# Kernel optimization log

Hardware: AMD Instinct MI355X
Metric: run time of the kernel (lower is better)

The kernel has to match this reference:

```python
import jax, jax.numpy as jnp
import numpy as np

N = 20000        # total nodes in batched graph
E = 160000       # edges (avg in-degree 8)
D_IN = 512
D_OUT = 512
MAX_DEG = 10
BN_EPS = 1e-5


def setup_inputs() -> dict:
    key = jax.random.key(0)
    ks = jax.random.split(key, 8)
    feats = jax.random.normal(ks[0], (N, D_IN), dtype=jnp.float32)
    src = jax.random.randint(ks[1], (E,), 0, N)
    dst = jax.random.randint(ks[2], (E,), 0, N)
    # Wl[d], bl[d]: lins_l for degree d (d>=1); Wl[0] is never used since h==0 for deg-0 nodes.
    # Wr[0], bl[0] play the role of lin_zero_deg; Wr[d] (d>=1) are the bias-free lins_r.
    Wl = jax.random.normal(ks[3], (MAX_DEG + 1, D_IN, D_OUT), dtype=jnp.float32) * 0.02
    Wr = jax.random.normal(ks[4], (MAX_DEG + 1, D_IN, D_OUT), dtype=jnp.float32) * 0.02
    bl = jax.random.normal(ks[5], (MAX_DEG + 1, D_OUT), dtype=jnp.float32) * 0.02
    gamma = jnp.ones((D_OUT,), dtype=jnp.float32)
    beta = jnp.zeros((D_OUT,), dtype=jnp.float32)
    return {"feats": feats, "src": src, "dst": dst, "Wl": Wl, "Wr": Wr,
            "bl": bl, "gamma": gamma, "beta": beta}


def reference(feats, src, dst, Wl, Wr, bl, gamma, beta):
    # 1) neighbor sum: h[v] = sum_{(u->v) in E} feats[u]   (fn.copy_u + fn.sum)
    h = jax.ops.segment_sum(feats[src], dst, num_segments=N)  # [N, D_IN]
    # in-degrees, clamped to max_degree
    deg = jnp.clip(jax.ops.segment_sum(jnp.ones((E,), dtype=jnp.int32), dst,
                                       num_segments=N), 0, MAX_DEG)  # [N]
    # 2) degree-bucketed linears, vectorized over the 11 buckets then gathered per node.
    #    out[n] = h[n] @ Wl[deg[n]] + feats[n] @ Wr[deg[n]] + bl[deg[n]]
    #    deg==0 nodes have h==0, so this reduces to lin_zero_deg(feats) = feats@Wr[0]+bl[0].
    Hl = jnp.einsum('ni,dio->dno', h, Wl)      # [11, N, D_OUT]
    Hr = jnp.einsum('ni,dio->dno', feats, Wr)  # [11, N, D_OUT]
    out = (Hl + Hr + bl[:, None, :])[deg, jnp.arange(N)]  # [N, D_OUT]
    # 3) batchnorm (training mode: batch stats, biased variance)
    mean = out.mean(axis=0)
    var = out.var(axis=0)
    out = (out - mean) * jax.lax.rsqrt(var + BN_EPS) * gamma + beta
    # 4) max aggregation over graph with self loops (fn.copy_u + fn.max)
    self_ids = jnp.arange(N)
    src_s = jnp.concatenate([src, self_ids])
    dst_s = jnp.concatenate([dst, self_ids])
    out = jax.ops.segment_max(out[src_s], dst_s, num_segments=N)  # [N, D_OUT]
    return out
```

## Files before the change

### kernel.cpp

```cpp
#include <hip/hip_runtime.h>
#include <hip/hip_bf16.h>
#include <stdint.h>

#define N_NODES 20000
#define N_EDGES 160000
#define DIN 512
#define DOUT 512
#define NBUCKET 11
#define KDIM 1024
#define MAXTILES 168
#define BN_EPS 1e-5f
#define CAP 64
#define CAST_BLOCKS (N_NODES / 4)
#define WT_BLOCKS ((KDIM / 32) * (DOUT / 32) * NBUCKET)
#define BUCKET_BLOCKS ((N_NODES + 255) / 256)

typedef float f32x4 __attribute__((ext_vector_type(4)));
typedef __attribute__((ext_vector_type(8))) __bf16 bf16x8;

static __device__ __forceinline__ unsigned short f2bf(float f) {
    union { float f; unsigned u; } v; v.f = f;
    unsigned r = v.u + 0x7FFFu + ((v.u >> 16) & 1u);
    return (unsigned short)(r >> 16);
}
static __device__ __forceinline__ float bflo(unsigned p) {
    union { unsigned u; float f; } v; v.u = p << 16; return v.f;
}
static __device__ __forceinline__ float bfhi(unsigned p) {
    union { unsigned u; float f; } v; v.u = p & 0xFFFF0000u; return v.f;
}
static __device__ __forceinline__ unsigned packbf(float lo, float hi) {
    return (unsigned)f2bf(lo) | ((unsigned)f2bf(hi) << 16);
}

static __device__ __forceinline__ void gload_lds16(const unsigned short* g, unsigned short* l) {
    __builtin_amdgcn_global_load_lds(
        (const __attribute__((address_space(1))) unsigned int*)g,
        (__attribute__((address_space(3))) unsigned int*)l, 16, 0, 0);
}

__global__ void k_scatter(const int* __restrict__ src, const int* __restrict__ dst,
                          int* __restrict__ cursor, int* __restrict__ eidx2) {
    int e = blockIdx.x * 256 + threadIdx.x;
    if (e >= N_EDGES) return;
    int v = dst[e];
    int slot = atomicAdd(&cursor[v], 1);
    if (slot < CAP) eidx2[v * CAP + slot] = src[e];
}

__global__ __launch_bounds__(256)
void k_prep(const float* __restrict__ feats, const float* __restrict__ Wl,
            const float* __restrict__ Wr, const int* __restrict__ cursor,
            unsigned short* __restrict__ X, unsigned short* __restrict__ Wt,
            int* __restrict__ bucket_cnt, int* __restrict__ bucket_nodes) {
    int b = blockIdx.x;
    int t = threadIdx.x;
    if (b < CAST_BLOCKS) {
        int n = b * 4 + (t >> 6);
        int col = (t & 63) * 8;
        f32x4 a = *(const f32x4*)(feats + (size_t)n * DIN + col);
        f32x4 c = *(const f32x4*)(feats + (size_t)n * DIN + col + 4);
        uint4 p;
        p.x = packbf(a[0], a[1]); p.y = packbf(a[2], a[3]);
        p.z = packbf(c[0], c[1]); p.w = packbf(c[2], c[3]);
        *(uint4*)(X + (size_t)n * KDIM + DIN + col) = p;
        return;
    }
    if (b < CAST_BLOCKS + WT_BLOCKS) {
        __shared__ float tile[32][33];
        int idx = b - CAST_BLOCKS;
        int d = idx / (32 * 16);
        int rem = idx % (32 * 16);
        int k0 = (rem & 31) * 32;
        int n0 = (rem >> 5) * 32;
        int c = t & 31, r0 = t >> 5;
        const float* srcp = (k0 < DIN) ? (Wl + (size_t)d * DIN * DOUT)
                                       : (Wr + (size_t)d * DIN * DOUT - (size_t)DIN * DOUT);
        for (int rr = 0; rr < 4; ++rr) {
            int r = r0 + rr * 8;
            tile[r][c] = srcp[(size_t)(k0 + r) * DOUT + n0 + c];
        }
        __syncthreads();
        for (int rr = 0; rr < 4; ++rr) {
            int r = r0 + rr * 8;
            Wt[((size_t)d * DOUT + n0 + r) * KDIM + k0 + c] = f2bf(tile[c][r]);
        }
        return;
    }
    __shared__ int lhist[NBUCKET];
    __shared__ int lbase[NBUCKET];
    if (t < NBUCKET) lhist[t] = 0;
    __syncthreads();
    int v = (b - CAST_BLOCKS - WT_BLOCKS) * 256 + t;
    int d = -1, slot = 0;
    if (v < N_NODES) {
        d = min(cursor[v], NBUCKET - 1);
        slot = atomicAdd(&lhist[d], 1);
    }
    __syncthreads();
    if (t < NBUCKET && lhist[t] > 0) lbase[t] = atomicAdd(&bucket_cnt[t], lhist[t]);
    __syncthreads();
    if (v < N_NODES) bucket_nodes[d * N_NODES + lbase[d] + slot] = v;
}

__global__ __launch_bounds__(256)
void k_build_x(const int* __restrict__ eidx2, const int* __restrict__ cursor,
               unsigned short* __restrict__ X) {
    int n = blockIdx.x * 4 + (threadIdx.x >> 6);
    int lane = threadIdx.x & 63;
    int col = lane * 8;
    int e = min(cursor[n], CAP);
    int av = eidx2[(size_t)n * CAP + lane];
    float acc[8] = {0,0,0,0,0,0,0,0};
    int i = 0;
    for (; i + 7 < e; i += 8) {
        uint4 p[8];
#pragma unroll
        for (int j = 0; j < 8; ++j) {
            int u = __shfl(av, i + j, 64);
            p[j] = *(const uint4*)(X + (size_t)u * KDIM + DIN + col);
        }
#pragma unroll
        for (int j = 0; j < 8; ++j) {
            acc[0] += bflo(p[j].x); acc[1] += bfhi(p[j].x);
            acc[2] += bflo(p[j].y); acc[3] += bfhi(p[j].y);
            acc[4] += bflo(p[j].z); acc[5] += bfhi(p[j].z);
            acc[6] += bflo(p[j].w); acc[7] += bfhi(p[j].w);
        }
    }
    if (i + 3 < e) {
        uint4 p[4];
#pragma unroll
        for (int j = 0; j < 4; ++j) {
            int u = __shfl(av, i + j, 64);
            p[j] = *(const uint4*)(X + (size_t)u * KDIM + DIN + col);
        }
#pragma unroll
        for (int j = 0; j < 4; ++j) {
            acc[0] += bflo(p[j].x); acc[1] += bfhi(p[j].x);
            acc[2] += bflo(p[j].y); acc[3] += bfhi(p[j].y);
            acc[4] += bflo(p[j].z); acc[5] += bfhi(p[j].z);
            acc[6] += bflo(p[j].w); acc[7] += bfhi(p[j].w);
        }
        i += 4;
    }
    for (; i < e; ++i) {
        int u = __shfl(av, i, 64);
        uint4 p = *(const uint4*)(X + (size_t)u * KDIM + DIN + col);
        acc[0] += bflo(p.x); acc[1] += bfhi(p.x); acc[2] += bflo(p.y); acc[3] += bfhi(p.y);
        acc[4] += bflo(p.z); acc[5] += bfhi(p.z); acc[6] += bflo(p.w); acc[7] += bfhi(p.w);
    }
    uint4 o;
    o.x = packbf(acc[0], acc[1]); o.y = packbf(acc[2], acc[3]);
    o.z = packbf(acc[4], acc[5]); o.w = packbf(acc[6], acc[7]);
    *(uint4*)(X + (size_t)n * KDIM + col) = o;
}

__global__ __launch_bounds__(256)
void k_gemm(const unsigned short* __restrict__ X, const unsigned short* __restrict__ Wt,
            const int* __restrict__ bucket_nodes, const int* __restrict__ bucket_cnt,
            const float* __restrict__ bl, unsigned short* __restrict__ out_pre,
            float* __restrict__ bn_sum, float* __restrict__ bn_sumsq) {
    int idx = blockIdx.x;
    int d = -1, m0 = 0, accum = 0, cnt = 0;
    for (int b = 0; b < NBUCKET; ++b) {
        int c = bucket_cnt[b];
        int nt = (c + 127) >> 7;
        if (d < 0 && idx < accum + nt) { d = b; m0 = (idx - accum) * 128; cnt = c; }
        accum += nt;
    }
    if (d < 0) return;
    int n0 = blockIdx.y * 128;

    __shared__ __align__(16) unsigned short As[128 * 64];
    __shared__ __align__(16) unsigned short Bs[128 * 64];
    __shared__ int ridS[128];
    __shared__ float colsum[128], colsq[128];

    int t = threadIdx.x;
    if (t < 128) {
        int gm = m0 + t;
        ridS[t] = (gm < cnt) ? bucket_nodes[d * N_NODES + gm] : -1;
        colsum[t] = 0.f; colsq[t] = 0.f;
    }
    __syncthreads();

    int lane = t & 63, w = t >> 6;
    int r = lane >> 3;
    int s = lane & 7;
    int sg = s ^ r;

    const unsigned short* gA[4];
    const unsigned short* gB[4];
    unsigned short* lA[4];
    unsigned short* lB[4];
#pragma unroll
    for (int j = 0; j < 4; ++j) {
        int row = w * 32 + j * 8 + r;
        int rid = max(ridS[row], 0);
        gA[j] = X + (size_t)rid * KDIM + sg * 8;
        gB[j] = Wt + ((size_t)d * DOUT + n0 + row) * KDIM + sg * 8;
        lA[j] = &As[(w * 32 + j * 8) * 64];
        lB[j] = &Bs[(w * 32 + j * 8) * 64];
    }

    int wm = (w & 1) * 64, wn = (w >> 1) * 64;
    int lm = lane & 15, q = lane >> 4;
    int sw = lm & 7;

    f32x4 acc[4][4];
#pragma unroll
    for (int i = 0; i < 4; ++i)
#pragma unroll
        for (int j = 0; j < 4; ++j) acc[i][j] = (f32x4){0, 0, 0, 0};

    for (int kt = 0; kt < KDIM / 64; ++kt) {
#pragma unroll
        for (int j = 0; j < 4; ++j) {
            gload_lds16(gA[j] + kt * 64, lA[j]);
            gload_lds16(gB[j] + kt * 64, lB[j]);
        }
        __syncthreads();

#pragma unroll
        for (int kk = 0; kk < 2; ++kk) {
            int slot = (kk * 4 + q) ^ sw;
            bf16x8 af[4], bfr[4];
#pragma unroll
            for (int mt = 0; mt < 4; ++mt)
                af[mt] = *(bf16x8*)&As[(wm + mt * 16 + lm) * 64 + slot * 8];
#pragma unroll
            for (int nt = 0; nt < 4; ++nt)
                bfr[nt] = *(bf16x8*)&Bs[(wn + nt * 16 + lm) * 64 + slot * 8];
#pragma unroll
            for (int mt = 0; mt < 4; ++mt)
#pragma unroll
                for (int nt = 0; nt < 4; ++nt)
                    acc[mt][nt] = __builtin_amdgcn_mfma_f32_16x16x32_bf16(af[mt], bfr[nt], acc[mt][nt], 0, 0, 0);
        }
        __syncthreads();
    }

    const float* blr = bl + d * DOUT + n0;
    float vsum[4] = {0, 0, 0, 0}, vsq[4] = {0, 0, 0, 0};
#pragma unroll
    for (int mt = 0; mt < 4; ++mt) {
#pragma unroll
        for (int rr = 0; rr < 4; ++rr) {
            int row = wm + mt * 16 + q * 4 + rr;
            int grow = ridS[row];
            if (grow < 0) continue;
            unsigned short* orow = out_pre + (size_t)grow * DOUT + n0;
#pragma unroll
            for (int nt = 0; nt < 4; ++nt) {
                int col = wn + nt * 16 + lm;
                float v = acc[mt][nt][rr] + blr[col];
                orow[col] = f2bf(v);
                vsum[nt] += v; vsq[nt] += v * v;
            }
        }
    }
#pragma unroll
    for (int nt = 0; nt < 4; ++nt) {
        vsum[nt] += __shfl_xor(vsum[nt], 16, 64);
        vsum[nt] += __shfl_xor(vsum[nt], 32, 64);
        vsq[nt]  += __shfl_xor(vsq[nt], 16, 64);
        vsq[nt]  += __shfl_xor(vsq[nt], 32, 64);
    }
    if (q == 0) {
#pragma unroll
        for (int nt = 0; nt < 4; ++nt) {
            atomicAdd(&colsum[wn + nt * 16 + lm], vsum[nt]);
            atomicAdd(&colsq[wn + nt * 16 + lm], vsq[nt]);
        }
    }
    __syncthreads();
    if (t < 128) {
        atomicAdd(&bn_sum[n0 + t], colsum[t]);
        atomicAdd(&bn_sumsq[n0 + t], colsq[t]);
    }
}

__global__ __launch_bounds__(256)
void k_max(const unsigned short* __restrict__ out_pre, const int* __restrict__ eidx2,
           const int* __restrict__ cursor, const float* __restrict__ bn_sum,
           const float* __restrict__ bn_sumsq, const float* __restrict__ gamma,
           const float* __restrict__ beta, float* __restrict__ out) {
    int n = blockIdx.x * 4 + (threadIdx.x >> 6);
    int lane = threadIdx.x & 63;
    int col = lane * 8;
    int e = min(cursor[n], CAP);
    int av = eidx2[(size_t)n * CAP + lane];
    float mx[8];
    {
        uint4 p = *(const uint4*)(out_pre + (size_t)n * DOUT + col);
        mx[0] = bflo(p.x); mx[1] = bfhi(p.x); mx[2] = bflo(p.y); mx[3] = bfhi(p.y);
        mx[4] = bflo(p.z); mx[5] = bfhi(p.z); mx[6] = bflo(p.w); mx[7] = bfhi(p.w);
    }
    int i = 0;
    for (; i + 7 < e; i += 8) {
        uint4 p[8];
#pragma unroll
        for (int j = 0; j < 8; ++j) {
            int u = __shfl(av, i + j, 64);
            p[j] = *(const uint4*)(out_pre + (size_t)u * DOUT + col);
        }
#pragma unroll
        for (int j = 0; j < 8; ++j) {
            mx[0] = fmaxf(mx[0], bflo(p[j].x)); mx[1] = fmaxf(mx[1], bfhi(p[j].x));
            mx[2] = fmaxf(mx[2], bflo(p[j].y)); mx[3] = fmaxf(mx[3], bfhi(p[j].y));
            mx[4] = fmaxf(mx[4], bflo(p[j].z)); mx[5] = fmaxf(mx[5], bfhi(p[j].z));
            mx[6] = fmaxf(mx[6], bflo(p[j].w)); mx[7] = fmaxf(mx[7], bfhi(p[j].w));
        }
    }
    if (i + 3 < e) {
        uint4 p[4];
#pragma unroll
        for (int j = 0; j < 4; ++j) {
            int u = __shfl(av, i + j, 64);
            p[j] = *(const uint4*)(out_pre + (size_t)u * DOUT + col);
        }
#pragma unroll
        for (int j = 0; j < 4; ++j) {
            mx[0] = fmaxf(mx[0], bflo(p[j].x)); mx[1] = fmaxf(mx[1], bfhi(p[j].x));
            mx[2] = fmaxf(mx[2], bflo(p[j].y)); mx[3] = fmaxf(mx[3], bfhi(p[j].y));
            mx[4] = fmaxf(mx[4], bflo(p[j].z)); mx[5] = fmaxf(mx[5], bfhi(p[j].z));
            mx[6] = fmaxf(mx[6], bflo(p[j].w)); mx[7] = fmaxf(mx[7], bfhi(p[j].w));
        }
        i += 4;
    }
    for (; i < e; ++i) {
        int u = __shfl(av, i, 64);
        uint4 p = *(const uint4*)(out_pre + (size_t)u * DOUT + col);
        mx[0] = fmaxf(mx[0], bflo(p.x)); mx[1] = fmaxf(mx[1], bfhi(p.x));
        mx[2] = fmaxf(mx[2], bflo(p.y)); mx[3] = fmaxf(mx[3], bfhi(p.y));
        mx[4] = fmaxf(mx[4], bflo(p.z)); mx[5] = fmaxf(mx[5], bfhi(p.z));
        mx[6] = fmaxf(mx[6], bflo(p.w)); mx[7] = fmaxf(mx[7], bfhi(p.w));
    }
    const float inv_n = 1.0f / (float)N_NODES;
    f32x4 sm0 = *(const f32x4*)(bn_sum + col);
    f32x4 sm1 = *(const f32x4*)(bn_sum + col + 4);
    f32x4 sq0 = *(const f32x4*)(bn_sumsq + col);
    f32x4 sq1 = *(const f32x4*)(bn_sumsq + col + 4);
    f32x4 g0 = *(const f32x4*)(gamma + col);
    f32x4 g1 = *(const f32x4*)(gamma + col + 4);
    f32x4 b0 = *(const f32x4*)(beta + col);
    f32x4 b1 = *(const f32x4*)(beta + col + 4);
    f32x4 r0, r1;
#pragma unroll
    for (int jj = 0; jj < 4; ++jj) {
        float mean = sm0[jj] * inv_n;
        float var = sq0[jj] * inv_n - mean * mean;
        float sc = g0[jj] * rsqrtf(var + BN_EPS);
        r0[jj] = mx[jj] * sc + (b0[jj] - mean * sc);
    }
#pragma unroll
    for (int jj = 0; jj < 4; ++jj) {
        float mean = sm1[jj] * inv_n;
        float var = sq1[jj] * inv_n - mean * mean;
        float sc = g1[jj] * rsqrtf(var + BN_EPS);
        r1[jj] = mx[jj + 4] * sc + (b1[jj] - mean * sc);
    }
    *(f32x4*)(out + (size_t)n * DOUT + col) = r0;
    *(f32x4*)(out + (size_t)n * DOUT + col + 4) = r1;
}

extern "C" void kernel_launch(void* const* d_in, const int* in_sizes, int n_in,
                              void* d_out, int out_size, void* d_ws, size_t ws_size,
                              hipStream_t stream) {
    const float* feats = (const float*)d_in[0];
    const int*   src   = (const int*)d_in[1];
    const int*   dst   = (const int*)d_in[2];
    const float* Wl    = (const float*)d_in[3];
    const float* Wr    = (const float*)d_in[4];
    const float* bl    = (const float*)d_in[5];
    const float* gamma = (const float*)d_in[6];
    const float* beta  = (const float*)d_in[7];
    float* out = (float*)d_out;

    char* ws = (char*)d_ws;
    size_t off = 0;
    auto alloc = [&](size_t bytes) -> void* {
        off = (off + 255) & ~(size_t)255;
        void* p = ws + off;
        off += bytes;
        return p;
    };

    int*   cursor     = (int*)alloc(N_NODES * 4);
    int*   bucket_cnt = (int*)alloc(16 * 4);
    float* bn_sum     = (float*)alloc(DOUT * 4);
    float* bn_sumsq   = (float*)alloc(DOUT * 4);
    size_t zbytes = off;

    int* bucket_nodes = (int*)alloc((size_t)NBUCKET * N_NODES * 4);
    int* eidx2        = (int*)alloc((size_t)N_NODES * CAP * 4);
    unsigned short* X  = (unsigned short*)alloc((size_t)N_NODES * KDIM * 2);
    unsigned short* Wt = (unsigned short*)alloc((size_t)NBUCKET * DOUT * KDIM * 2);
    unsigned short* out_pre = (unsigned short*)alloc((size_t)N_NODES * DOUT * 2);

    hipMemsetAsync(d_ws, 0, zbytes, stream);

    k_scatter<<<(N_EDGES + 255) / 256, 256, 0, stream>>>(src, dst, cursor, eidx2);
    k_prep<<<CAST_BLOCKS + WT_BLOCKS + BUCKET_BLOCKS, 256, 0, stream>>>(
        feats, Wl, Wr, cursor, X, Wt, bucket_cnt, bucket_nodes);
    k_build_x<<<N_NODES / 4, 256, 0, stream>>>(eidx2, cursor, X);
    k_gemm<<<dim3(MAXTILES, 4), 256, 0, stream>>>(
        X, Wt, bucket_nodes, bucket_cnt, bl, out_pre, bn_sum, bn_sumsq);
    k_max<<<N_NODES / 4, 256, 0, stream>>>(out_pre, eidx2, cursor, bn_sum, bn_sumsq, gamma, beta, out);
}
```

Baseline: 218.8 us.

## Shrink GEMM N-tile to 64 and remap blocks for grouped L2 reuse

The bucketed GEMM now uses 128x64 output tiles instead of 128x128, which doubles the block count to fill more compute units. The launch is flattened to a 1D grid where groups of 8 consecutive blocks share the same N-column slice across different M tiles, and each run of 64 blocks covers all 8 N slices for 8 M tiles, which should improve L2 reuse of the weight and activation tiles. In exchange, each block has lower arithmetic intensity: every A element is loaded twice as often overall, and each wave holds a 64x32 sub-tile.

```diff
diff --git a/kernel.cpp b/kernel.cpp
--- a/kernel.cpp
+++ b/kernel.cpp
@@ -14,6 +14,7 @@
 #define CAST_BLOCKS (N_NODES / 4)
 #define WT_BLOCKS ((KDIM / 32) * (DOUT / 32) * NBUCKET)
 #define BUCKET_BLOCKS ((N_NODES + 255) / 256)
+#define GEMM_BLOCKS (8 * MAXTILES)
 
 typedef float f32x4 __attribute__((ext_vector_type(4)));
 typedef __attribute__((ext_vector_type(8))) __bf16 bf16x8;
@@ -161,99 +162,103 @@
             const int* __restrict__ bucket_nodes, const int* __restrict__ bucket_cnt,
             const float* __restrict__ bl, unsigned short* __restrict__ out_pre,
             float* __restrict__ bn_sum, float* __restrict__ bn_sumsq) {
-    int idx = blockIdx.x;
+    int b = blockIdx.x;
+    int tile = (b & 7) + ((b >> 6) << 3);
+    int n0 = ((b >> 3) & 7) * 64;
     int d = -1, m0 = 0, accum = 0, cnt = 0;
-    for (int b = 0; b < NBUCKET; ++b) {
-        int c = bucket_cnt[b];
+    for (int bb = 0; bb < NBUCKET; ++bb) {
+        int c = bucket_cnt[bb];
         int nt = (c + 127) >> 7;
-        if (d < 0 && idx < accum + nt) { d = b; m0 = (idx - accum) * 128; cnt = c; }
+        if (d < 0 && tile < accum + nt) { d = bb; m0 = (tile - accum) * 128; cnt = c; }
         accum += nt;
     }
     if (d < 0) return;
-    int n0 = blockIdx.y * 128;
 
     __shared__ __align__(16) unsigned short As[128 * 64];
-    __shared__ __align__(16) unsigned short Bs[128 * 64];
+    __shared__ __align__(16) unsigned short Bs[64 * 64];
     __shared__ int ridS[128];
-    __shared__ float colsum[128], colsq[128];
+    __shared__ float colsum[64], colsq[64];
 
     int t = threadIdx.x;
     if (t < 128) {
         int gm = m0 + t;
         ridS[t] = (gm < cnt) ? bucket_nodes[d * N_NODES + gm] : -1;
-        colsum[t] = 0.f; colsq[t] = 0.f;
+        if (t < 64) { colsum[t] = 0.f; colsq[t] = 0.f; }
     }
     __syncthreads();
 
     int lane = t & 63, w = t >> 6;
-    int r = lane >> 3;
-    int s = lane & 7;
-    int sg = s ^ r;
+    int sr = t >> 3;
+    int s = t & 7;
+    int sg = s ^ (sr & 7);
 
     const unsigned short* gA[4];
-    const unsigned short* gB[4];
+    const unsigned short* gB[2];
     unsigned short* lA[4];
-    unsigned short* lB[4];
+    unsigned short* lB[2];
 #pragma unroll
     for (int j = 0; j < 4; ++j) {
-        int row = w * 32 + j * 8 + r;
+        int row = j * 32 + sr;
         int rid = max(ridS[row], 0);
         gA[j] = X + (size_t)rid * KDIM + sg * 8;
+        lA[j] = &As[row * 64 + s * 8];
+    }
+#pragma unroll
+    for (int j = 0; j < 2; ++j) {
+        int row = j * 32 + sr;
         gB[j] = Wt + ((size_t)d * DOUT + n0 + row) * KDIM + sg * 8;
-        lA[j] = &As[(w * 32 + j * 8) * 64];
-        lB[j] = &Bs[(w * 32 + j * 8) * 64];
-    }
-
-    int wm = (w & 1) * 64, wn = (w >> 1) * 64;
+        lB[j] = &Bs[row * 64 + s * 8];
+    }
+
+    int wr = w >> 1, wc = w & 1;
     int lm = lane & 15, q = lane >> 4;
     int sw = lm & 7;
 
-    f32x4 acc[4][4];
+    f32x4 acc[4][2];
 #pragma unroll
     for (int i = 0; i < 4; ++i)
 #pragma unroll
-        for (int j = 0; j < 4; ++j) acc[i][j] = (f32x4){0, 0, 0, 0};
+        for (int j = 0; j < 2; ++j) acc[i][j] = (f32x4){0, 0, 0, 0};
 
     for (int kt = 0; kt < KDIM / 64; ++kt) {
 #pragma unroll
-        for (int j = 0; j < 4; ++j) {
-            gload_lds16(gA[j] + kt * 64, lA[j]);
-            gload_lds16(gB[j] + kt * 64, lB[j]);
-        }
+        for (int j = 0; j < 4; ++j) gload_lds16(gA[j] + kt * 64, lA[j]);
+#pragma unroll
+        for (int j = 0; j < 2; ++j) gload_lds16(gB[j] + kt * 64, lB[j]);
         __syncthreads();
 
 #pragma unroll
         for (int kk = 0; kk < 2; ++kk) {
             int slot = (kk * 4 + q) ^ sw;
-            bf16x8 af[4], bfr[4];
+            bf16x8 af[4], bfr[2];
 #pragma unroll
             for (int mt = 0; mt < 4; ++mt)
-                af[mt] = *(bf16x8*)&As[(wm + mt * 16 + lm) * 64 + slot * 8];
-#pragma unroll
-            for (int nt = 0; nt < 4; ++nt)
-                bfr[nt] = *(bf16x8*)&Bs[(wn + nt * 16 + lm) * 64 + slot * 8];
+                af[mt] = *(bf16x8*)&As[(wr * 64 + mt * 16 + lm) * 64 + slot * 8];
+#pragma unroll
+            for (int nt = 0; nt < 2; ++nt)
+                bfr[nt] = *(bf16x8*)&Bs[(wc * 32 + nt * 16 + lm) * 64 + slot * 8];
 #pragma unroll
             for (int mt = 0; mt < 4; ++mt)
 #pragma unroll
-                for (int nt = 0; nt < 4; ++nt)
+                for (int nt = 0; nt < 2; ++nt)
                     acc[mt][nt] = __builtin_amdgcn_mfma_f32_16x16x32_bf16(af[mt], bfr[nt], acc[mt][nt], 0, 0, 0);
         }
         __syncthreads();
     }
 
     const float* blr = bl + d * DOUT + n0;
-    float vsum[4] = {0, 0, 0, 0}, vsq[4] = {0, 0, 0, 0};
+    float vsum[2] = {0, 0}, vsq[2] = {0, 0};
 #pragma unroll
     for (int mt = 0; mt < 4; ++mt) {
 #pragma unroll
         for (int rr = 0; rr < 4; ++rr) {
-            int row = wm + mt * 16 + q * 4 + rr;
+            int row = wr * 64 + mt * 16 + q * 4 + rr;
             int grow = ridS[row];
             if (grow < 0) continue;
             unsigned short* orow = out_pre + (size_t)grow * DOUT + n0;
 #pragma unroll
-            for (int nt = 0; nt < 4; ++nt) {
-                int col = wn + nt * 16 + lm;
+            for (int nt = 0; nt < 2; ++nt) {
+                int col = wc * 32 + nt * 16 + lm;
                 float v = acc[mt][nt][rr] + blr[col];
                 orow[col] = f2bf(v);
                 vsum[nt] += v; vsq[nt] += v * v;
@@ -261,7 +266,7 @@
         }
     }
 #pragma unroll
-    for (int nt = 0; nt < 4; ++nt) {
+    for (int nt = 0; nt < 2; ++nt) {
         vsum[nt] += __shfl_xor(vsum[nt], 16, 64);
         vsum[nt] += __shfl_xor(vsum[nt], 32, 64);
         vsq[nt]  += __shfl_xor(vsq[nt], 16, 64);
@@ -269,13 +274,13 @@
     }
     if (q == 0) {
 #pragma unroll
-        for (int nt = 0; nt < 4; ++nt) {
-            atomicAdd(&colsum[wn + nt * 16 + lm], vsum[nt]);
-            atomicAdd(&colsq[wn + nt * 16 + lm], vsq[nt]);
+        for (int nt = 0; nt < 2; ++nt) {
+            atomicAdd(&colsum[wc * 32 + nt * 16 + lm], vsum[nt]);
+            atomicAdd(&colsq[wc * 32 + nt * 16 + lm], vsq[nt]);
         }
     }
     __syncthreads();
-    if (t < 128) {
+    if (t < 64) {
         atomicAdd(&bn_sum[n0 + t], colsum[t]);
         atomicAdd(&bn_sumsq[n0 + t], colsq[t]);
     }
@@ -405,7 +410,7 @@
     k_prep<<<CAST_BLOCKS + WT_BLOCKS + BUCKET_BLOCKS, 256, 0, stream>>>(
         feats, Wl, Wr, cursor, X, Wt, bucket_cnt, bucket_nodes);
     k_build_x<<<N_NODES / 4, 256, 0, stream>>>(eidx2, cursor, X);
-    k_gemm<<<dim3(MAXTILES, 4), 256, 0, stream>>>(
+    k_gemm<<<GEMM_BLOCKS, 256, 0, stream>>>(
         X, Wt, bucket_nodes, bucket_cnt, bl, out_pre, bn_sum, bn_sumsq);
     k_max<<<N_NODES / 4, 256, 0, stream>>>(out_pre, eidx2, cursor, bn_sum, bn_sumsq, gamma, beta, out);
 }
```

New measurement: 218.2 us. Within noise of the previous version (-0.3%).
